# Performance work log

Hardware: AMD Instinct MI355X
Metric: run time of the kernel (lower is better)

## Reference

```python
import jax, jax.numpy as jnp
import numpy as np

EPS = 1e-06

def _feature_map(x):
    # elu(x) + 1 -> strictly positive feature map
    return jax.nn.elu(x) + 1.0

def setup_inputs() -> dict:
    key = jax.random.key(0)
    kq, kk, kv = jax.random.split(key, 3)
    B, H, N, D = 1, 16, 2048, 64
    Q = jax.random.normal(kq, (B, H, N, D), dtype=jnp.float32)
    K = jax.random.normal(kk, (B, H, N, D), dtype=jnp.float32)
    V = jax.random.normal(kv, (B, H, N, D), dtype=jnp.float32)
    return {"Q": Q, "K": K, "V": V, "causal": 1}

def reference(Q, K, V, causal):
    Qf = _feature_map(Q)  # (B,H,N,D)
    Kf = _feature_map(K)  # (B,H,N,D)
    if causal:
        # prefix sums of per-position outer products K_m V_m^T  -> (B,H,N,D,Dv)
        KV_prefix = jnp.cumsum(Kf[..., :, None] * V[..., None, :], axis=2)
        Kf_prefix = jnp.cumsum(Kf, axis=2)  # (B,H,N,D)
        num = jnp.einsum('bhnd,bhnde->bhne', Qf, KV_prefix)
        den = jnp.einsum('bhnd,bhnd->bhn', Qf, Kf_prefix)[..., None]
        return num / (den + EPS)
    else:
        KV = jnp.einsum('bhnd,bhne->bhde', Kf, V)            # (B,H,D,Dv)
        num = jnp.einsum('bhnd,bhde->bhne', Qf, KV)          # (B,H,N,Dv)
        den = jnp.einsum('bhnd,bhd->bhn', Qf, Kf.sum(axis=2))[..., None]
        return num / (den + EPS)
```

## Files before the change

### kernel.cpp

```cpp
#include <hip/hip_runtime.h>

#define Hh   16
#define Nn   2048
#define Dd   64
#define DVv  64
#define Ll   64
#define Cc   (Nn / Ll)
#define HCc  (Hh * Cc)
#define EPSf 1e-6f
#define LDP  72

typedef __attribute__((ext_vector_type(8))) __bf16 bf16x8;
typedef __attribute__((ext_vector_type(4))) __bf16 bf16x4;
typedef __attribute__((ext_vector_type(4))) float  f32x4;

__device__ __forceinline__ float fmap(float x) {
    return x > 0.0f ? (x + 1.0f) : __expf(x);
}
__device__ __forceinline__ __bf16 tobf(float x) { return (__bf16)x; }

__global__ __launch_bounds__(256) void k_chunk_sums(
    const float* __restrict__ Kg, const float* __restrict__ Vg,
    __bf16* __restrict__ SwsT, float* __restrict__ zws)
{
    __shared__ __align__(16) __bf16 sKT[Dd][LDP];
    __shared__ __align__(16) __bf16 sVT[80][LDP];
    const int t  = threadIdx.x;
    const int hc = blockIdx.x;
    const float4* K4 = (const float4*)(Kg + (size_t)hc * (Ll * Dd));
    const float4* V4 = (const float4*)(Vg + (size_t)hc * (Ll * DVv));
    for (int i = t; i < (Ll * Dd) / 4; i += 256) {
        float4 k4 = K4[i];
        float4 v4 = V4[i];
        const int m  = i >> 4;
        const int c0 = (i & 15) * 4;
        sKT[c0 + 0][m] = tobf(fmap(k4.x));
        sKT[c0 + 1][m] = tobf(fmap(k4.y));
        sKT[c0 + 2][m] = tobf(fmap(k4.z));
        sKT[c0 + 3][m] = tobf(fmap(k4.w));
        sVT[c0 + 0][m] = tobf(v4.x);
        sVT[c0 + 1][m] = tobf(v4.y);
        sVT[c0 + 2][m] = tobf(v4.z);
        sVT[c0 + 3][m] = tobf(v4.w);
    }
    for (int i = t; i < 16 * LDP; i += 256) {
        const int r = i / LDP, c = i % LDP;
        sVT[64 + r][c] = (r == 0) ? (__bf16)1.0f : (__bf16)0.0f;
    }
    __syncthreads();

    const int lane = t & 63, wv = t >> 6;
    const int col = lane & 15, quad = lane >> 4;
    __bf16* So = SwsT + (size_t)hc * (Dd * DVv);
    for (int et = 0; et < 5; ++et) {
        f32x4 acc = {0.f, 0.f, 0.f, 0.f};
#pragma unroll
        for (int ks = 0; ks < 2; ++ks) {
            bf16x8 a = *(const bf16x8*)&sKT[wv * 16 + col][ks * 32 + quad * 8];
            bf16x8 b = *(const bf16x8*)&sVT[et * 16 + col][ks * 32 + quad * 8];
            acc = __builtin_amdgcn_mfma_f32_16x16x32_bf16(a, b, acc, 0, 0, 0);
        }
        if (et < 4) {
            const int e = et * 16 + col;
            const int d = wv * 16 + quad * 4;
            bf16x4 s4 = { tobf(acc[0]), tobf(acc[1]), tobf(acc[2]), tobf(acc[3]) };
            *(bf16x4*)&So[e * Dd + d] = s4;
        } else if (col == 0) {
#pragma unroll
            for (int j = 0; j < 4; ++j)
                zws[hc * Dd + wv * 16 + quad * 4 + j] = acc[j];
        }
    }
}

__global__ __launch_bounds__(256) void k_output(
    const float* __restrict__ Qg, const float* __restrict__ Kg,
    const float* __restrict__ Vg, const __bf16* __restrict__ SwsT,
    const float* __restrict__ zws, float* __restrict__ Og)
{
    __shared__ __align__(16) __bf16 aQ[Ll][LDP];
    __shared__ __align__(16) __bf16 aK[Ll][LDP];
    __shared__ __align__(16) __bf16 sW[Ll][LDP];
    __shared__ __align__(16) __bf16 bV[80][LDP];
    __shared__ __align__(16) __bf16 bS[80][LDP];
    const int t  = threadIdx.x;
    const int hc = blockIdx.x;
    const int h  = hc >> 5, c = hc & 31;
    const int lane = t & 63, wv = t >> 6;
    const int col = lane & 15, quad = lane >> 4;

    {
        const float4* Q4 = (const float4*)(Qg + (size_t)hc * (Ll * Dd));
        const float4* K4 = (const float4*)(Kg + (size_t)hc * (Ll * Dd));
        const float4* V4 = (const float4*)(Vg + (size_t)hc * (Ll * DVv));
        for (int i = t; i < (Ll * Dd) / 4; i += 256) {
            float4 q4 = Q4[i];
            float4 k4 = K4[i];
            float4 v4 = V4[i];
            const int m  = i >> 4;
            const int c0 = (i & 15) * 4;
            bf16x4 qv = { tobf(fmap(q4.x)), tobf(fmap(q4.y)), tobf(fmap(q4.z)), tobf(fmap(q4.w)) };
            bf16x4 kv = { tobf(fmap(k4.x)), tobf(fmap(k4.y)), tobf(fmap(k4.z)), tobf(fmap(k4.w)) };
            *(bf16x4*)&aQ[m][c0] = qv;
            *(bf16x4*)&aK[m][c0] = kv;
            bV[c0 + 0][m] = tobf(v4.x);
            bV[c0 + 1][m] = tobf(v4.y);
            bV[c0 + 2][m] = tobf(v4.z);
            bV[c0 + 3][m] = tobf(v4.w);
        }
        for (int i = t; i < 16 * LDP; i += 256) {
            const int r = i / LDP, cc = i % LDP;
            bV[64 + r][cc] = (r == 0) ? (__bf16)1.0f : (__bf16)0.0f;
        }
    }

    {
        const __bf16* Sb = SwsT + ((size_t)(h * Cc)) * (Dd * DVv) + t * 16;
        float racc[16];
#pragma unroll
        for (int j = 0; j < 16; ++j) racc[j] = 0.0f;
        for (int cc = 0; cc < c; ++cc) {
            bf16x8 s0 = *(const bf16x8*)(Sb + (size_t)cc * (Dd * DVv));
            bf16x8 s1 = *(const bf16x8*)(Sb + (size_t)cc * (Dd * DVv) + 8);
#pragma unroll
            for (int j = 0; j < 8; ++j) { racc[j] += (float)s0[j]; racc[8 + j] += (float)s1[j]; }
        }
        const int e = t >> 2, d0 = (t & 3) * 16;
#pragma unroll
        for (int j = 0; j < 16; ++j) bS[e][d0 + j] = tobf(racc[j]);

        if (t < Dd) {
            const float* zb = zws + (h * Cc) * Dd + t;
            float zr = 0.0f;
            for (int cc = 0; cc < c; ++cc) zr += zb[cc * Dd];
            bS[64][t] = tobf(zr);
        }
        for (int i = t; i < 16 * LDP; i += 256) {
            const int r = i / LDP, cc = i % LDP;
            if (!(r == 0 && cc < Dd)) bS[64 + r][cc] = (__bf16)0.0f;
        }
    }
    __syncthreads();

#pragma unroll 1
    for (int mt = 0; mt < 4; ++mt) {
        f32x4 wacc = {0.f, 0.f, 0.f, 0.f};
#pragma unroll
        for (int ks = 0; ks < 2; ++ks) {
            bf16x8 a = *(const bf16x8*)&aQ[wv * 16 + col][ks * 32 + quad * 8];
            bf16x8 b = *(const bf16x8*)&aK[mt * 16 + col][ks * 32 + quad * 8];
            wacc = __builtin_amdgcn_mfma_f32_16x16x32_bf16(a, b, wacc, 0, 0, 0);
        }
#pragma unroll
        for (int j = 0; j < 4; ++j) {
            const int n = wv * 16 + quad * 4 + j;
            const int m = mt * 16 + col;
            sW[n][m] = tobf(m <= n ? wacc[j] : 0.0f);
        }
    }
    __syncthreads();

    f32x4 accs[5];
#pragma unroll 1
    for (int et = 0; et < 5; ++et) {
        f32x4 acc = {0.f, 0.f, 0.f, 0.f};
#pragma unroll
        for (int ks = 0; ks < 2; ++ks) {
            bf16x8 a = *(const bf16x8*)&sW[wv * 16 + col][ks * 32 + quad * 8];
            bf16x8 b = *(const bf16x8*)&bV[et * 16 + col][ks * 32 + quad * 8];
            acc = __builtin_amdgcn_mfma_f32_16x16x32_bf16(a, b, acc, 0, 0, 0);
        }
#pragma unroll
        for (int ks = 0; ks < 2; ++ks) {
            bf16x8 a = *(const bf16x8*)&aQ[wv * 16 + col][ks * 32 + quad * 8];
            bf16x8 b = *(const bf16x8*)&bS[et * 16 + col][ks * 32 + quad * 8];
            acc = __builtin_amdgcn_mfma_f32_16x16x32_bf16(a, b, acc, 0, 0, 0);
        }
        accs[et] = acc;
    }
    float dn[4];
#pragma unroll
    for (int j = 0; j < 4; ++j) dn[j] = __shfl(accs[4][j], lane & 48);

    float* Oc = Og + (size_t)hc * (Ll * DVv);
#pragma unroll
    for (int et = 0; et < 4; ++et) {
#pragma unroll
        for (int j = 0; j < 4; ++j) {
            const int n = wv * 16 + quad * 4 + j;
            Oc[n * DVv + et * 16 + col] = accs[et][j] / (dn[j] + EPSf);
        }
    }
}

extern "C" void kernel_launch(void* const* d_in, const int* in_sizes, int n_in,
                              void* d_out, int out_size, void* d_ws, size_t ws_size,
                              hipStream_t stream) {
    const float* Q = (const float*)d_in[0];
    const float* K = (const float*)d_in[1];
    const float* V = (const float*)d_in[2];
    __bf16* SwsT = (__bf16*)d_ws;
    float*  zws  = (float*)((char*)d_ws + (size_t)HCc * Dd * DVv * sizeof(__bf16));
    float* out = (float*)d_out;

    k_chunk_sums<<<HCc, 256, 0, stream>>>(K, V, SwsT, zws);
    k_output<<<HCc, 256, 0, stream>>>(Q, K, V, SwsT, zws, out);
}
```

Before: 95.07 us.

## Add separate exclusive-prefix-scan kernel over chunk state sums

Adds a k_prefix kernel that turns the per-chunk KV outer-product sums and key sums into exclusive prefix sums in place. k_output then loads one precomputed state per chunk instead of re-summing up to 31 previous chunk states per block, which removes the quadratic redundant global reads. The cost is a third kernel launch with only 36 blocks, a serial 32-step scan per thread, and an extra bf16 rounding of the running state at every chunk.

```diff
diff --git a/kernel.cpp b/kernel.cpp
--- a/kernel.cpp
+++ b/kernel.cpp
@@ -73,6 +73,54 @@
     }
 }
 
+__global__ __launch_bounds__(256) void k_prefix(
+    __bf16* __restrict__ SwsT, float* __restrict__ zws)
+{
+    const int b = blockIdx.x, t = threadIdx.x;
+    if (b < 32) {
+        const int gid = b * 256 + t;
+        const int h   = gid >> 9;
+        const int sl  = gid & 511;
+        __bf16* base = SwsT + ((size_t)h * Cc) * (Dd * DVv) + sl * 8;
+        float run[8];
+#pragma unroll
+        for (int j = 0; j < 8; ++j) run[j] = 0.0f;
+#pragma unroll
+        for (int cb = 0; cb < 4; ++cb) {
+            bf16x8 v[8];
+#pragma unroll
+            for (int k = 0; k < 8; ++k)
+                v[k] = *(const bf16x8*)(base + (size_t)(cb * 8 + k) * (Dd * DVv));
+#pragma unroll
+            for (int k = 0; k < 8; ++k) {
+                bf16x8 o;
+#pragma unroll
+                for (int j = 0; j < 8; ++j) {
+                    o[j] = tobf(run[j]);
+                    run[j] += (float)v[k][j];
+                }
+                *(bf16x8*)(base + (size_t)(cb * 8 + k) * (Dd * DVv)) = o;
+            }
+        }
+    } else {
+        const int gid = (b - 32) * 256 + t;
+        const int h = gid >> 6, d = gid & 63;
+        float* zb = zws + (h * Cc) * Dd + d;
+        float run = 0.0f;
+#pragma unroll
+        for (int cb = 0; cb < 4; ++cb) {
+            float v[8];
+#pragma unroll
+            for (int k = 0; k < 8; ++k) v[k] = zb[(cb * 8 + k) * Dd];
+#pragma unroll
+            for (int k = 0; k < 8; ++k) {
+                zb[(cb * 8 + k) * Dd] = run;
+                run += v[k];
+            }
+        }
+    }
+}
+
 __global__ __launch_bounds__(256) void k_output(
     const float* __restrict__ Qg, const float* __restrict__ Kg,
     const float* __restrict__ Vg, const __bf16* __restrict__ SwsT,
@@ -85,7 +133,6 @@
     __shared__ __align__(16) __bf16 bS[80][LDP];
     const int t  = threadIdx.x;
     const int hc = blockIdx.x;
-    const int h  = hc >> 5, c = hc & 31;
     const int lane = t & 63, wv = t >> 6;
     const int col = lane & 15, quad = lane >> 4;
 
@@ -115,26 +162,13 @@
     }
 
     {
-        const __bf16* Sb = SwsT + ((size_t)(h * Cc)) * (Dd * DVv) + t * 16;
-        float racc[16];
-#pragma unroll
-        for (int j = 0; j < 16; ++j) racc[j] = 0.0f;
-        for (int cc = 0; cc < c; ++cc) {
-            bf16x8 s0 = *(const bf16x8*)(Sb + (size_t)cc * (Dd * DVv));
-            bf16x8 s1 = *(const bf16x8*)(Sb + (size_t)cc * (Dd * DVv) + 8);
-#pragma unroll
-            for (int j = 0; j < 8; ++j) { racc[j] += (float)s0[j]; racc[8 + j] += (float)s1[j]; }
-        }
-        const int e = t >> 2, d0 = (t & 3) * 16;
-#pragma unroll
-        for (int j = 0; j < 16; ++j) bS[e][d0 + j] = tobf(racc[j]);
-
-        if (t < Dd) {
-            const float* zb = zws + (h * Cc) * Dd + t;
-            float zr = 0.0f;
-            for (int cc = 0; cc < c; ++cc) zr += zb[cc * Dd];
-            bS[64][t] = tobf(zr);
-        }
+        const __bf16* Sp = SwsT + (size_t)hc * (Dd * DVv);
+        for (int i = t; i < (Dd * DVv) / 8; i += 256) {
+            bf16x8 s = *(const bf16x8*)(Sp + i * 8);
+            const int e = i >> 3, d0 = (i & 7) * 8;
+            *(bf16x8*)&bS[e][d0] = s;
+        }
+        if (t < Dd) bS[64][t] = tobf(zws[hc * Dd + t]);
         for (int i = t; i < 16 * LDP; i += 256) {
             const int r = i / LDP, cc = i % LDP;
             if (!(r == 0 && cc < Dd)) bS[64 + r][cc] = (__bf16)0.0f;
@@ -204,5 +238,6 @@
     float* out = (float*)d_out;
 
     k_chunk_sums<<<HCc, 256, 0, stream>>>(K, V, SwsT, zws);
+    k_prefix<<<36, 256, 0, stream>>>(SwsT, zws);
     k_output<<<HCc, 256, 0, stream>>>(Q, K, V, SwsT, zws, out);
 }
```

Result: faster. 88.78 us, median of 2 (-6.6%).

## Add a dedicated prefix-scan kernel over chunk states and cache bf16 K/V

Applied to the files above, without the earlier changes.

The chunk-state sums now go through a separate exclusive prefix-scan kernel. Before, each output block re-summed all preceding chunk states, a quadratic amount of redundant reads. The normaliser z is packed as row 64 of each state, and the first kernel also writes feature-mapped K and transposed V in bf16 so the output kernel copies them instead of reloading fp32 and recomputing. This adds a third launch and extra workspace traffic, and the running sum is stored in bf16 per chunk.

```diff
diff --git a/kernel.cpp b/kernel.cpp
--- a/kernel.cpp
+++ b/kernel.cpp
@@ -7,6 +7,7 @@
 #define Ll   64
 #define Cc   (Nn / Ll)
 #define HCc  (Hh * Cc)
+#define CS   (65 * 64)
 #define EPSf 1e-6f
 #define LDP  72
 
@@ -21,7 +22,8 @@
 
 __global__ __launch_bounds__(256) void k_chunk_sums(
     const float* __restrict__ Kg, const float* __restrict__ Vg,
-    __bf16* __restrict__ SwsT, float* __restrict__ zws)
+    __bf16* __restrict__ Sws, __bf16* __restrict__ Kfb,
+    __bf16* __restrict__ Vtb)
 {
     __shared__ __align__(16) __bf16 sKT[Dd][LDP];
     __shared__ __align__(16) __bf16 sVT[80][LDP];
@@ -29,15 +31,18 @@
     const int hc = blockIdx.x;
     const float4* K4 = (const float4*)(Kg + (size_t)hc * (Ll * Dd));
     const float4* V4 = (const float4*)(Vg + (size_t)hc * (Ll * DVv));
+    __bf16* Kfo = Kfb + (size_t)hc * (Ll * Dd);
     for (int i = t; i < (Ll * Dd) / 4; i += 256) {
         float4 k4 = K4[i];
         float4 v4 = V4[i];
         const int m  = i >> 4;
         const int c0 = (i & 15) * 4;
-        sKT[c0 + 0][m] = tobf(fmap(k4.x));
-        sKT[c0 + 1][m] = tobf(fmap(k4.y));
-        sKT[c0 + 2][m] = tobf(fmap(k4.z));
-        sKT[c0 + 3][m] = tobf(fmap(k4.w));
+        bf16x4 kv = { tobf(fmap(k4.x)), tobf(fmap(k4.y)), tobf(fmap(k4.z)), tobf(fmap(k4.w)) };
+        sKT[c0 + 0][m] = kv[0];
+        sKT[c0 + 1][m] = kv[1];
+        sKT[c0 + 2][m] = kv[2];
+        sKT[c0 + 3][m] = kv[3];
+        *(bf16x4*)&Kfo[m * Dd + c0] = kv;
         sVT[c0 + 0][m] = tobf(v4.x);
         sVT[c0 + 1][m] = tobf(v4.y);
         sVT[c0 + 2][m] = tobf(v4.z);
@@ -51,7 +56,7 @@
 
     const int lane = t & 63, wv = t >> 6;
     const int col = lane & 15, quad = lane >> 4;
-    __bf16* So = SwsT + (size_t)hc * (Dd * DVv);
+    __bf16* So = Sws + (size_t)hc * CS;
     for (int et = 0; et < 5; ++et) {
         f32x4 acc = {0.f, 0.f, 0.f, 0.f};
 #pragma unroll
@@ -60,23 +65,54 @@
             bf16x8 b = *(const bf16x8*)&sVT[et * 16 + col][ks * 32 + quad * 8];
             acc = __builtin_amdgcn_mfma_f32_16x16x32_bf16(a, b, acc, 0, 0, 0);
         }
+        bf16x4 s4 = { tobf(acc[0]), tobf(acc[1]), tobf(acc[2]), tobf(acc[3]) };
+        const int d = wv * 16 + quad * 4;
         if (et < 4) {
-            const int e = et * 16 + col;
-            const int d = wv * 16 + quad * 4;
-            bf16x4 s4 = { tobf(acc[0]), tobf(acc[1]), tobf(acc[2]), tobf(acc[3]) };
-            *(bf16x4*)&So[e * Dd + d] = s4;
+            *(bf16x4*)&So[(et * 16 + col) * Dd + d] = s4;
         } else if (col == 0) {
-#pragma unroll
-            for (int j = 0; j < 4; ++j)
-                zws[hc * Dd + wv * 16 + quad * 4 + j] = acc[j];
+            *(bf16x4*)&So[64 * Dd + d] = s4;
+        }
+    }
+    __bf16* Vto = Vtb + (size_t)hc * (Ll * DVv);
+    for (int i = t; i < (Ll * DVv) / 8; i += 256) {
+        const int e = i >> 3, m0 = (i & 7) * 8;
+        *(bf16x8*)&Vto[e * Ll + m0] = *(const bf16x8*)&sVT[e][m0];
+    }
+}
+
+__global__ __launch_bounds__(256) void k_prefix(__bf16* __restrict__ Sws)
+{
+    const int gid = blockIdx.x * 256 + threadIdx.x;
+    if (gid >= Hh * (CS / 8)) return;
+    const int h  = gid / (CS / 8);
+    const int sl = gid % (CS / 8);
+    __bf16* base = Sws + (size_t)h * Cc * CS + sl * 8;
+    float run[8];
+#pragma unroll
+    for (int j = 0; j < 8; ++j) run[j] = 0.0f;
+#pragma unroll
+    for (int cb = 0; cb < 4; ++cb) {
+        bf16x8 v[8];
+#pragma unroll
+        for (int k = 0; k < 8; ++k)
+            v[k] = *(const bf16x8*)(base + (size_t)(cb * 8 + k) * CS);
+#pragma unroll
+        for (int k = 0; k < 8; ++k) {
+            bf16x8 o;
+#pragma unroll
+            for (int j = 0; j < 8; ++j) {
+                o[j] = tobf(run[j]);
+                run[j] += (float)v[k][j];
+            }
+            *(bf16x8*)(base + (size_t)(cb * 8 + k) * CS) = o;
         }
     }
 }
 
 __global__ __launch_bounds__(256) void k_output(
-    const float* __restrict__ Qg, const float* __restrict__ Kg,
-    const float* __restrict__ Vg, const __bf16* __restrict__ SwsT,
-    const float* __restrict__ zws, float* __restrict__ Og)
+    const float* __restrict__ Qg, const __bf16* __restrict__ Kfb,
+    const __bf16* __restrict__ Vtb, const __bf16* __restrict__ Sws,
+    float* __restrict__ Og)
 {
     __shared__ __align__(16) __bf16 aQ[Ll][LDP];
     __shared__ __align__(16) __bf16 aK[Ll][LDP];
@@ -85,59 +121,36 @@
     __shared__ __align__(16) __bf16 bS[80][LDP];
     const int t  = threadIdx.x;
     const int hc = blockIdx.x;
-    const int h  = hc >> 5, c = hc & 31;
     const int lane = t & 63, wv = t >> 6;
     const int col = lane & 15, quad = lane >> 4;
 
     {
         const float4* Q4 = (const float4*)(Qg + (size_t)hc * (Ll * Dd));
-        const float4* K4 = (const float4*)(Kg + (size_t)hc * (Ll * Dd));
-        const float4* V4 = (const float4*)(Vg + (size_t)hc * (Ll * DVv));
         for (int i = t; i < (Ll * Dd) / 4; i += 256) {
             float4 q4 = Q4[i];
-            float4 k4 = K4[i];
-            float4 v4 = V4[i];
             const int m  = i >> 4;
             const int c0 = (i & 15) * 4;
             bf16x4 qv = { tobf(fmap(q4.x)), tobf(fmap(q4.y)), tobf(fmap(q4.z)), tobf(fmap(q4.w)) };
-            bf16x4 kv = { tobf(fmap(k4.x)), tobf(fmap(k4.y)), tobf(fmap(k4.z)), tobf(fmap(k4.w)) };
             *(bf16x4*)&aQ[m][c0] = qv;
-            *(bf16x4*)&aK[m][c0] = kv;
-            bV[c0 + 0][m] = tobf(v4.x);
-            bV[c0 + 1][m] = tobf(v4.y);
-            bV[c0 + 2][m] = tobf(v4.z);
-            bV[c0 + 3][m] = tobf(v4.w);
+        }
+    }
+    {
+        const __bf16* Kfo = Kfb + (size_t)hc * (Ll * Dd);
+        const __bf16* Vto = Vtb + (size_t)hc * (Ll * DVv);
+        const __bf16* Sp  = Sws + (size_t)hc * CS;
+        for (int i = t; i < (Ll * Dd) / 8; i += 256) {
+            const int r = i >> 3, c0 = (i & 7) * 8;
+            *(bf16x8*)&aK[r][c0] = *(const bf16x8*)(Kfo + i * 8);
+            *(bf16x8*)&bV[r][c0] = *(const bf16x8*)(Vto + i * 8);
+        }
+        for (int i = t; i < CS / 8; i += 256) {
+            const int r = i >> 3, c0 = (i & 7) * 8;
+            *(bf16x8*)&bS[r][c0] = *(const bf16x8*)(Sp + i * 8);
         }
         for (int i = t; i < 16 * LDP; i += 256) {
             const int r = i / LDP, cc = i % LDP;
             bV[64 + r][cc] = (r == 0) ? (__bf16)1.0f : (__bf16)0.0f;
-        }
-    }
-
-    {
-        const __bf16* Sb = SwsT + ((size_t)(h * Cc)) * (Dd * DVv) + t * 16;
-        float racc[16];
-#pragma unroll
-        for (int j = 0; j < 16; ++j) racc[j] = 0.0f;
-        for (int cc = 0; cc < c; ++cc) {
-            bf16x8 s0 = *(const bf16x8*)(Sb + (size_t)cc * (Dd * DVv));
-            bf16x8 s1 = *(const bf16x8*)(Sb + (size_t)cc * (Dd * DVv) + 8);
-#pragma unroll
-            for (int j = 0; j < 8; ++j) { racc[j] += (float)s0[j]; racc[8 + j] += (float)s1[j]; }
-        }
-        const int e = t >> 2, d0 = (t & 3) * 16;
-#pragma unroll
-        for (int j = 0; j < 16; ++j) bS[e][d0 + j] = tobf(racc[j]);
-
-        if (t < Dd) {
-            const float* zb = zws + (h * Cc) * Dd + t;
-            float zr = 0.0f;
-            for (int cc = 0; cc < c; ++cc) zr += zb[cc * Dd];
-            bS[64][t] = tobf(zr);
-        }
-        for (int i = t; i < 16 * LDP; i += 256) {
-            const int r = i / LDP, cc = i % LDP;
-            if (!(r == 0 && cc < Dd)) bS[64 + r][cc] = (__bf16)0.0f;
+            if (r > 0) bS[64 + r][cc] = (__bf16)0.0f;
         }
     }
     __syncthreads();
@@ -199,10 +212,13 @@
     const float* Q = (const float*)d_in[0];
     const float* K = (const float*)d_in[1];
     const float* V = (const float*)d_in[2];
-    __bf16* SwsT = (__bf16*)d_ws;
-    float*  zws  = (float*)((char*)d_ws + (size_t)HCc * Dd * DVv * sizeof(__bf16));
+    unsigned char* ws = (unsigned char*)d_ws;
+    __bf16* Sws = (__bf16*)ws;
+    __bf16* Kfb = (__bf16*)(ws + (size_t)HCc * CS * 2);
+    __bf16* Vtb = Kfb + (size_t)HCc * Ll * Dd;
     float* out = (float*)d_out;
 
-    k_chunk_sums<<<HCc, 256, 0, stream>>>(K, V, SwsT, zws);
-    k_output<<<HCc, 256, 0, stream>>>(Q, K, V, SwsT, zws, out);
-}
+    k_chunk_sums<<<HCc, 256, 0, stream>>>(K, V, Sws, Kfb, Vtb);
+    k_prefix<<<(Hh * (CS / 8) + 255) / 256, 256, 0, stream>>>(Sws);
+    k_output<<<HCc, 256, 0, stream>>>(Q, Kfb, Vtb, Sws, out);
+}
```

Result: faster. 89.66 us (-5.7%).
